# Kernel tuning notes

Hardware: AMD Instinct MI355X
Metric: run time of the kernel (lower is better)

## Reference

```python
import jax, jax.numpy as jnp
import numpy as np

B, H, KVH, D, S, NSLOTS = 16, 32, 8, 128, 4096, 131072
BASE = 10000.0
SCALE = 1.0 / float(np.sqrt(D))


def _rope(x, pos, inv_freq):
    # x: [..., D]; pos broadcastable to x.shape[:-1]
    freqs = pos[..., None].astype(jnp.float32) * inv_freq  # [..., D//2]
    emb = jnp.concatenate([freqs, freqs], axis=-1)         # [..., D]
    cos, sin = jnp.cos(emb), jnp.sin(emb)
    x1, x2 = x[..., : D // 2], x[..., D // 2:]
    rotated = jnp.concatenate([-x2, x1], axis=-1)
    return x * cos + rotated * sin


def setup_inputs() -> dict:
    key = jax.random.key(0)
    k1, k2, k3, k4, k5, k6 = jax.random.split(key, 6)
    query = jax.random.normal(k1, (B, H, D), dtype=jnp.float32)
    k_cache = jax.random.normal(k2, (NSLOTS, KVH, D), dtype=jnp.float32)
    v_cache = jax.random.normal(k3, (NSLOTS, KVH, D), dtype=jnp.float32)
    slots = jax.random.randint(k4, (B, S), 0, NSLOTS, dtype=jnp.int32)
    positions = jnp.sort(jax.random.randint(k5, (B, S), 0, 4096, dtype=jnp.int32), axis=-1)
    context_lens = jax.random.randint(k6, (B,), 1, S + 1, dtype=jnp.int32)
    return {"query": query, "k_cache": k_cache, "v_cache": v_cache,
            "slots": slots, "positions": positions, "context_lens": context_lens}


def reference(query, k_cache, v_cache, slots, positions, context_lens):
    inv_freq = 1.0 / (BASE ** (jnp.arange(0, D, 2, dtype=jnp.float32) / D))  # [D//2]
    # paged gather of non-contiguous KV slots
    K = jnp.transpose(k_cache[slots], (0, 2, 1, 3))  # [B, KVH, S, D]
    V = jnp.transpose(v_cache[slots], (0, 2, 1, 3))  # [B, KVH, S, D]
    # rotary: keys at their cached positions, query at last valid position
    Kr = _rope(K, positions[:, None, :], inv_freq)                       # [B,KVH,S,D]
    pos_last = jnp.take_along_axis(positions, (context_lens - 1)[:, None], axis=1)  # [B,1]
    qr = _rope(query, pos_last, inv_freq)                                # [B,H,D]
    # GQA: group query heads over shared KV heads
    G = H // KVH
    qg = qr.reshape(B, KVH, G, D)
    scores = jnp.einsum('bhgd,bhsd->bhgs', qg, Kr) * SCALE               # [B,KVH,G,S]
    valid = jnp.arange(S, dtype=jnp.int32)[None, None, None, :] < context_lens[:, None, None, None]
    scores = jnp.where(valid, scores, jnp.float32(-1e30))
    attn = jax.nn.softmax(scores, axis=-1)
    out = jnp.einsum('bhgs,bhsd->bhgd', attn, V).reshape(B, H, D)
    return out
```

## Files before the change

kernel.cpp:

```cpp
#include <hip/hip_runtime.h>
#include <math.h>

#define BB 16
#define HH 32
#define KVHH 8
#define GG 4
#define DD 128
#define SS 4096
#define PGROUPS 64
#define SPAN (SS / PGROUPS)
#define PSTRIDE (GG * DD + 2 * GG)
#define SCALE 0.08838834764831845f

__global__ __launch_bounds__(256) void pa_split(
    const float* __restrict__ q,
    const float* __restrict__ kc,
    const float* __restrict__ vc,
    const int* __restrict__ slots,
    const int* __restrict__ positions,
    const int* __restrict__ ctxlen,
    float* __restrict__ part)
{
  const int blk  = blockIdx.x;
  const int sub  = blk & 7;
  const int bkv  = blk >> 3;
  const int b    = bkv >> 3;
  const int kvh  = bkv & 7;
  const int tid  = threadIdx.x;
  const int lane = tid & 31;
  const int grp  = tid >> 5;
  const int p    = sub * 8 + grp;
  const int s0   = p * SPAN;
  const int ctx  = ctxlen[b];
  int nvalid = ctx - s0;
  nvalid = nvalid < 0 ? 0 : (nvalid > SPAN ? SPAN : nvalid);

  const int d0 = lane * 4;
  float invf[4];
  #pragma unroll
  for (int i = 0; i < 4; ++i) {
    int j = (d0 + i) & 63;
    invf[i] = __expf(-0.14391156f * (float)j);
  }

  const int pos_last = positions[b * SS + (ctx - 1)];
  float qsn[4], qcs[4];
  #pragma unroll
  for (int i = 0; i < 4; ++i) {
    __sincosf((float)pos_last * invf[i], &qsn[i], &qcs[i]);
  }
  float qr[GG][4];
  #pragma unroll
  for (int g = 0; g < GG; ++g) {
    const float4 x4 = *(const float4*)(q + ((size_t)b * HH + kvh * GG + g) * DD + d0);
    float x[4] = {x4.x, x4.y, x4.z, x4.w};
    #pragma unroll
    for (int i = 0; i < 4; ++i) {
      float px = __shfl_xor(x[i], 16, 32);
      float r  = (lane < 16) ? -px : px;
      qr[g][i] = (x[i] * qcs[i] + r * qsn[i]) * SCALE;
    }
  }

  const int sbase = b * SS + s0;
  const int slotA = slots[sbase + lane];
  const int slotB = slots[sbase + 32 + lane];
  const int posA  = positions[sbase + lane];
  const int posB  = positions[sbase + 32 + lane];

  float m[GG], l[GG], acc[GG][4];
  #pragma unroll
  for (int g = 0; g < GG; ++g) {
    m[g] = -1e30f; l[g] = 0.f;
    #pragma unroll
    for (int i = 0; i < 4; ++i) acc[g][i] = 0.f;
  }

  float4 k4, v4;
  int pos_cur = 0;
  if (nvalid > 0) {
    int slot = __shfl(slotA, 0, 32);
    pos_cur  = __shfl(posA, 0, 32);
    const size_t roff = ((size_t)slot * KVHH + kvh) * DD + d0;
    k4 = *(const float4*)(kc + roff);
    v4 = *(const float4*)(vc + roff);
  }

  for (int it = 0; it < nvalid; ++it) {
    float4 nk4 = k4, nv4 = v4;
    int pos_nxt = 0;
    if (it + 1 < nvalid) {
      const int i1 = it + 1;
      int slot = (i1 < 32) ? __shfl(slotA, i1, 32) : __shfl(slotB, i1 - 32, 32);
      pos_nxt  = (i1 < 32) ? __shfl(posA, i1, 32) : __shfl(posB, i1 - 32, 32);
      const size_t roff = ((size_t)slot * KVHH + kvh) * DD + d0;
      nk4 = *(const float4*)(kc + roff);
      nv4 = *(const float4*)(vc + roff);
    }

    float kx[4] = {k4.x, k4.y, k4.z, k4.w};
    float kr[4];
    #pragma unroll
    for (int i = 0; i < 4; ++i) {
      float pk = __shfl_xor(kx[i], 16, 32);
      float r  = (lane < 16) ? -pk : pk;
      float sn, cs;
      __sincosf((float)pos_cur * invf[i], &sn, &cs);
      kr[i] = kx[i] * cs + r * sn;
    }

    float sc[GG];
    #pragma unroll
    for (int g = 0; g < GG; ++g)
      sc[g] = qr[g][0]*kr[0] + qr[g][1]*kr[1] + qr[g][2]*kr[2] + qr[g][3]*kr[3];
    #pragma unroll
    for (int off = 16; off > 0; off >>= 1) {
      #pragma unroll
      for (int g = 0; g < GG; ++g)
        sc[g] += __shfl_xor(sc[g], off, 32);
    }

    float vx[4] = {v4.x, v4.y, v4.z, v4.w};
    #pragma unroll
    for (int g = 0; g < GG; ++g) {
      float mn   = fmaxf(m[g], sc[g]);
      float corr = __expf(m[g] - mn);
      float pw   = __expf(sc[g] - mn);
      l[g] = l[g] * corr + pw;
      #pragma unroll
      for (int i = 0; i < 4; ++i)
        acc[g][i] = acc[g][i] * corr + pw * vx[i];
      m[g] = mn;
    }

    k4 = nk4; v4 = nv4; pos_cur = pos_nxt;
  }

  float* pb = part + ((size_t)bkv * PGROUPS + p) * PSTRIDE;
  #pragma unroll
  for (int g = 0; g < GG; ++g) {
    *(float4*)(pb + g * DD + d0) =
        make_float4(acc[g][0], acc[g][1], acc[g][2], acc[g][3]);
  }
  if (lane == 0) {
    #pragma unroll
    for (int g = 0; g < GG; ++g) {
      pb[GG * DD + g]      = m[g];
      pb[GG * DD + GG + g] = l[g];
    }
  }
}

__global__ __launch_bounds__(128) void pa_combine(
    const float* __restrict__ part, float* __restrict__ out)
{
  const int bh  = blockIdx.x;
  const int b   = bh >> 5;
  const int h   = bh & 31;
  const int kvh = h >> 2;
  const int g   = h & 3;
  const int d   = threadIdx.x;

  const float* pbase = part + ((size_t)(b * KVHH + kvh)) * PGROUPS * PSTRIDE;
  float M = -1e30f, L = 0.f, o = 0.f;
  for (int p = 0; p < PGROUPS; ++p) {
    const float* pp = pbase + (size_t)p * PSTRIDE;
    float mp = pp[GG * DD + g];
    float lp = pp[GG * DD + GG + g];
    float a  = pp[g * DD + d];
    float Mn = fmaxf(M, mp);
    float e0 = __expf(M - Mn);
    float e1 = __expf(mp - Mn);
    o = o * e0 + a * e1;
    L = L * e0 + lp * e1;
    M = Mn;
  }
  out[((size_t)b * HH + h) * DD + d] = o / L;
}

extern "C" void kernel_launch(void* const* d_in, const int* in_sizes, int n_in,
                              void* d_out, int out_size, void* d_ws, size_t ws_size,
                              hipStream_t stream) {
  const float* q_p   = (const float*)d_in[0];
  const float* kc_p  = (const float*)d_in[1];
  const float* vc_p  = (const float*)d_in[2];
  const int*   slots = (const int*)d_in[3];
  const int*   poss  = (const int*)d_in[4];
  const int*   ctxl  = (const int*)d_in[5];
  float* part = (float*)d_ws;
  float* outp = (float*)d_out;

  pa_split<<<BB * KVHH * (PGROUPS / 8), 256, 0, stream>>>(
      q_p, kc_p, vc_p, slots, poss, ctxl, part);
  pa_combine<<<BB * HH, 128, 0, stream>>>(part, outp);
}
```

Baseline: 856.0 us.

## Split paged attention into two-pass K scoring and V accumulation with dynamic chunking

Each warp now covers a span sized to the actual context length, so every split group gets roughly equal work and no warp idles past the valid tokens. Scores are computed in a first pass over K with double-buffered batches of four gathered rows, stored in shared memory, and softmaxed exactly. A second pass then gathers V, also double-buffered, and accumulates weighted sums without the per-token rescaling of the online softmax. When the workspace is large enough it uses 128 partitions, which doubles the combine work and the partial-result traffic.

```diff
diff --git a/kernel.cpp b/kernel.cpp
--- a/kernel.cpp
+++ b/kernel.cpp
@@ -7,11 +7,10 @@
 #define GG 4
 #define DD 128
 #define SS 4096
-#define PGROUPS 64
-#define SPAN (SS / PGROUPS)
 #define PSTRIDE (GG * DD + 2 * GG)
 #define SCALE 0.08838834764831845f
 
+template<int PG>
 __global__ __launch_bounds__(256) void pa_split(
     const float* __restrict__ q,
     const float* __restrict__ kc,
@@ -21,19 +20,24 @@
     const int* __restrict__ ctxlen,
     float* __restrict__ part)
 {
+  constexpr int NSUB = PG / 8;
+  constexpr int CH   = SS / PG;
+  __shared__ float smem[8][CH][GG];
+
   const int blk  = blockIdx.x;
-  const int sub  = blk & 7;
-  const int bkv  = blk >> 3;
+  const int sub  = blk % NSUB;
+  const int bkv  = blk / NSUB;
   const int b    = bkv >> 3;
   const int kvh  = bkv & 7;
   const int tid  = threadIdx.x;
   const int lane = tid & 31;
   const int grp  = tid >> 5;
   const int p    = sub * 8 + grp;
-  const int s0   = p * SPAN;
   const int ctx  = ctxlen[b];
+  const int chunk = (ctx + PG - 1) / PG;
+  const int s0   = p * chunk;
   int nvalid = ctx - s0;
-  nvalid = nvalid < 0 ? 0 : (nvalid > SPAN ? SPAN : nvalid);
+  nvalid = nvalid < 0 ? 0 : (nvalid > chunk ? chunk : nvalid);
 
   const int d0 = lane * 4;
   float invf[4];
@@ -46,9 +50,8 @@
   const int pos_last = positions[b * SS + (ctx - 1)];
   float qsn[4], qcs[4];
   #pragma unroll
-  for (int i = 0; i < 4; ++i) {
+  for (int i = 0; i < 4; ++i)
     __sincosf((float)pos_last * invf[i], &qsn[i], &qcs[i]);
-  }
   float qr[GG][4];
   #pragma unroll
   for (int g = 0; g < GG; ++g) {
@@ -64,93 +67,162 @@
 
   const int sbase = b * SS + s0;
   const int slotA = slots[sbase + lane];
-  const int slotB = slots[sbase + 32 + lane];
   const int posA  = positions[sbase + lane];
-  const int posB  = positions[sbase + 32 + lane];
-
-  float m[GG], l[GG], acc[GG][4];
-  #pragma unroll
-  for (int g = 0; g < GG; ++g) {
-    m[g] = -1e30f; l[g] = 0.f;
+  int slotB = 0, posB = 0;
+  if constexpr (CH == 64) {
+    slotB = slots[sbase + 32 + lane];
+    posB  = positions[sbase + 32 + lane];
+  }
+  auto SLOT = [&](int it) {
+    if constexpr (CH == 64)
+      return (it < 32) ? __shfl(slotA, it, 32) : __shfl(slotB, it - 32, 32);
+    else
+      return __shfl(slotA, it, 32);
+  };
+  auto POS = [&](int it) {
+    if constexpr (CH == 64)
+      return (it < 32) ? __shfl(posA, it, 32) : __shfl(posB, it - 32, 32);
+    else
+      return __shfl(posA, it, 32);
+  };
+
+  auto LOADK = [&](float4 (&kb)[4], int base) {
+    #pragma unroll
+    for (int j = 0; j < 4; ++j) {
+      int it = base + j;
+      if (it < nvalid) {
+        int slot = SLOT(it);
+        kb[j] = *(const float4*)(kc + ((size_t)slot * KVHH + kvh) * DD + d0);
+      }
+    }
+  };
+  auto COMPK = [&](float4 (&kb)[4], int base) {
+    #pragma unroll
+    for (int j = 0; j < 4; ++j) {
+      int it = base + j;
+      if (it < nvalid) {
+        int pos = POS(it);
+        float kx[4] = {kb[j].x, kb[j].y, kb[j].z, kb[j].w};
+        float sc0 = 0.f, sc1 = 0.f, sc2 = 0.f, sc3 = 0.f;
+        #pragma unroll
+        for (int i = 0; i < 4; ++i) {
+          float pk = __shfl_xor(kx[i], 16, 32);
+          float r  = (lane < 16) ? -pk : pk;
+          float sn, cs;
+          __sincosf((float)pos * invf[i], &sn, &cs);
+          float kr = kx[i] * cs + r * sn;
+          sc0 += qr[0][i] * kr;
+          sc1 += qr[1][i] * kr;
+          sc2 += qr[2][i] * kr;
+          sc3 += qr[3][i] * kr;
+        }
+        #pragma unroll
+        for (int off = 16; off > 0; off >>= 1) {
+          sc0 += __shfl_xor(sc0, off, 32);
+          sc1 += __shfl_xor(sc1, off, 32);
+          sc2 += __shfl_xor(sc2, off, 32);
+          sc3 += __shfl_xor(sc3, off, 32);
+        }
+        if (lane < 4) {
+          float v = lane == 0 ? sc0 : lane == 1 ? sc1 : lane == 2 ? sc2 : sc3;
+          smem[grp][it][lane] = v;
+        }
+      }
+    }
+  };
+
+  float4 bufA[4], bufB[4];
+  LOADK(bufA, 0);
+  for (int base = 0; base < nvalid; base += 8) {
+    LOADK(bufB, base + 4);
+    COMPK(bufA, base);
+    LOADK(bufA, base + 8);
+    COMPK(bufB, base + 4);
+  }
+
+  const int g2 = lane & 3;
+  const int t0 = lane >> 2;
+  float mx = -1e30f;
+  #pragma unroll
+  for (int k = 0; k < CH / 8; ++k) {
+    int it = t0 + 8 * k;
+    if (it < nvalid) mx = fmaxf(mx, smem[grp][it][g2]);
+  }
+  mx = fmaxf(mx, __shfl_xor(mx, 4, 32));
+  mx = fmaxf(mx, __shfl_xor(mx, 8, 32));
+  mx = fmaxf(mx, __shfl_xor(mx, 16, 32));
+  float ls = 0.f;
+  #pragma unroll
+  for (int k = 0; k < CH / 8; ++k) {
+    int it = t0 + 8 * k;
+    if (it < nvalid) {
+      float w = __expf(smem[grp][it][g2] - mx);
+      smem[grp][it][g2] = w;
+      ls += w;
+    }
+  }
+  ls += __shfl_xor(ls, 4, 32);
+  ls += __shfl_xor(ls, 8, 32);
+  ls += __shfl_xor(ls, 16, 32);
+
+  float acc[GG][4];
+  #pragma unroll
+  for (int g = 0; g < GG; ++g)
     #pragma unroll
     for (int i = 0; i < 4; ++i) acc[g][i] = 0.f;
-  }
-
-  float4 k4, v4;
-  int pos_cur = 0;
-  if (nvalid > 0) {
-    int slot = __shfl(slotA, 0, 32);
-    pos_cur  = __shfl(posA, 0, 32);
-    const size_t roff = ((size_t)slot * KVHH + kvh) * DD + d0;
-    k4 = *(const float4*)(kc + roff);
-    v4 = *(const float4*)(vc + roff);
-  }
-
-  for (int it = 0; it < nvalid; ++it) {
-    float4 nk4 = k4, nv4 = v4;
-    int pos_nxt = 0;
-    if (it + 1 < nvalid) {
-      const int i1 = it + 1;
-      int slot = (i1 < 32) ? __shfl(slotA, i1, 32) : __shfl(slotB, i1 - 32, 32);
-      pos_nxt  = (i1 < 32) ? __shfl(posA, i1, 32) : __shfl(posB, i1 - 32, 32);
-      const size_t roff = ((size_t)slot * KVHH + kvh) * DD + d0;
-      nk4 = *(const float4*)(kc + roff);
-      nv4 = *(const float4*)(vc + roff);
-    }
-
-    float kx[4] = {k4.x, k4.y, k4.z, k4.w};
-    float kr[4];
-    #pragma unroll
-    for (int i = 0; i < 4; ++i) {
-      float pk = __shfl_xor(kx[i], 16, 32);
-      float r  = (lane < 16) ? -pk : pk;
-      float sn, cs;
-      __sincosf((float)pos_cur * invf[i], &sn, &cs);
-      kr[i] = kx[i] * cs + r * sn;
-    }
-
-    float sc[GG];
-    #pragma unroll
-    for (int g = 0; g < GG; ++g)
-      sc[g] = qr[g][0]*kr[0] + qr[g][1]*kr[1] + qr[g][2]*kr[2] + qr[g][3]*kr[3];
-    #pragma unroll
-    for (int off = 16; off > 0; off >>= 1) {
-      #pragma unroll
-      for (int g = 0; g < GG; ++g)
-        sc[g] += __shfl_xor(sc[g], off, 32);
-    }
-
-    float vx[4] = {v4.x, v4.y, v4.z, v4.w};
-    #pragma unroll
-    for (int g = 0; g < GG; ++g) {
-      float mn   = fmaxf(m[g], sc[g]);
-      float corr = __expf(m[g] - mn);
-      float pw   = __expf(sc[g] - mn);
-      l[g] = l[g] * corr + pw;
-      #pragma unroll
-      for (int i = 0; i < 4; ++i)
-        acc[g][i] = acc[g][i] * corr + pw * vx[i];
-      m[g] = mn;
-    }
-
-    k4 = nk4; v4 = nv4; pos_cur = pos_nxt;
-  }
-
-  float* pb = part + ((size_t)bkv * PGROUPS + p) * PSTRIDE;
-  #pragma unroll
-  for (int g = 0; g < GG; ++g) {
+
+  auto LOADV = [&](float4 (&vb)[4], int base) {
+    #pragma unroll
+    for (int j = 0; j < 4; ++j) {
+      int it = base + j;
+      if (it < nvalid) {
+        int slot = SLOT(it);
+        vb[j] = *(const float4*)(vc + ((size_t)slot * KVHH + kvh) * DD + d0);
+      }
+    }
+  };
+  auto COMPV = [&](float4 (&vb)[4], int base) {
+    #pragma unroll
+    for (int j = 0; j < 4; ++j) {
+      int it = base + j;
+      if (it < nvalid) {
+        float w0 = smem[grp][it][0];
+        float w1 = smem[grp][it][1];
+        float w2 = smem[grp][it][2];
+        float w3 = smem[grp][it][3];
+        float4 v4 = vb[j];
+        acc[0][0] += w0 * v4.x; acc[0][1] += w0 * v4.y;
+        acc[0][2] += w0 * v4.z; acc[0][3] += w0 * v4.w;
+        acc[1][0] += w1 * v4.x; acc[1][1] += w1 * v4.y;
+        acc[1][2] += w1 * v4.z; acc[1][3] += w1 * v4.w;
+        acc[2][0] += w2 * v4.x; acc[2][1] += w2 * v4.y;
+        acc[2][2] += w2 * v4.z; acc[2][3] += w2 * v4.w;
+        acc[3][0] += w3 * v4.x; acc[3][1] += w3 * v4.y;
+        acc[3][2] += w3 * v4.z; acc[3][3] += w3 * v4.w;
+      }
+    }
+  };
+
+  LOADV(bufA, 0);
+  for (int base = 0; base < nvalid; base += 8) {
+    LOADV(bufB, base + 4);
+    COMPV(bufA, base);
+    LOADV(bufA, base + 8);
+    COMPV(bufB, base + 4);
+  }
+
+  float* pb = part + ((size_t)bkv * PG + p) * PSTRIDE;
+  #pragma unroll
+  for (int g = 0; g < GG; ++g)
     *(float4*)(pb + g * DD + d0) =
         make_float4(acc[g][0], acc[g][1], acc[g][2], acc[g][3]);
-  }
-  if (lane == 0) {
-    #pragma unroll
-    for (int g = 0; g < GG; ++g) {
-      pb[GG * DD + g]      = m[g];
-      pb[GG * DD + GG + g] = l[g];
-    }
+  if (lane < 4) {
+    pb[GG * DD + lane]      = mx;
+    pb[GG * DD + GG + lane] = ls;
   }
 }
 
+template<int PG>
 __global__ __launch_bounds__(128) void pa_combine(
     const float* __restrict__ part, float* __restrict__ out)
 {
@@ -161,9 +233,9 @@
   const int g   = h & 3;
   const int d   = threadIdx.x;
 
-  const float* pbase = part + ((size_t)(b * KVHH + kvh)) * PGROUPS * PSTRIDE;
+  const float* pbase = part + ((size_t)(b * KVHH + kvh)) * PG * PSTRIDE;
   float M = -1e30f, L = 0.f, o = 0.f;
-  for (int p = 0; p < PGROUPS; ++p) {
+  for (int p = 0; p < PG; ++p) {
     const float* pp = pbase + (size_t)p * PSTRIDE;
     float mp = pp[GG * DD + g];
     float lp = pp[GG * DD + GG + g];
@@ -190,7 +262,14 @@
   float* part = (float*)d_ws;
   float* outp = (float*)d_out;
 
-  pa_split<<<BB * KVHH * (PGROUPS / 8), 256, 0, stream>>>(
-      q_p, kc_p, vc_p, slots, poss, ctxl, part);
-  pa_combine<<<BB * HH, 128, 0, stream>>>(part, outp);
+  const size_t need128 = (size_t)BB * KVHH * 128 * PSTRIDE * sizeof(float);
+  if (ws_size >= need128) {
+    pa_split<128><<<BB * KVHH * 16, 256, 0, stream>>>(
+        q_p, kc_p, vc_p, slots, poss, ctxl, part);
+    pa_combine<128><<<BB * HH, 128, 0, stream>>>(part, outp);
+  } else {
+    pa_split<64><<<BB * KVHH * 8, 256, 0, stream>>>(
+        q_p, kc_p, vc_p, slots, poss, ctxl, part);
+    pa_combine<64><<<BB * HH, 128, 0, stream>>>(part, outp);
+  }
 }
```

New measurement: 860.2 us. About the same (+0.5%).
